# Kernel tuning notes

Measured on AMD Instinct MI355X. Metric: run time of the kernel, lower is better.

Reference implementation:

```python
import jax, jax.numpy as jnp
import numpy as np

EPS = 1e-7  # Keras binary_crossentropy epsilon


def setup_inputs() -> dict:
    key = jax.random.key(0)
    ks = jax.random.split(key, 4)
    B, D, H = 256, 512, 512
    return {
        "embeddings": jax.random.normal(ks[0], (B, D), dtype=jnp.float32),
        "labels": jax.random.randint(ks[1], (B,), 0, 16),
        "W1": jax.random.normal(ks[2], (2 * D, H), dtype=jnp.float32) / np.float32(np.sqrt(2 * D)),
        "b1": jnp.zeros((H,), jnp.float32),
        "W2": jax.random.normal(ks[3], (H, 1), dtype=jnp.float32) / np.float32(np.sqrt(H)),
        "b2": jnp.zeros((1,), jnp.float32),
    }


def reference(embeddings, labels, W1, b1, W2, b2):
    # All-pairs expansion equivalent to tf.meshgrid + tf.gather over batch indices.
    # Pair (i, j): input1 = embeddings[j] (fast axis), input2 = embeddings[i].
    B, D = embeddings.shape
    x1 = jnp.broadcast_to(embeddings[None, :, :], (B, B, D))
    x2 = jnp.broadcast_to(embeddings[:, None, :], (B, B, D))
    x = jnp.concatenate([x1, x2], axis=-1)  # (B, B, 2D)
    # metric_layer: siamese dense head -> pairwise similarity probability
    h = jax.nn.relu(jnp.einsum('ijd,dh->ijh', x, W1) + b1)          # (B, B, H)
    p = jax.nn.sigmoid(jnp.einsum('ijh,ho->ijo', h, W2) + b2)[..., 0]  # (B, B)
    p = jnp.clip(p, EPS, 1.0 - EPS)
    # target_function: label equality (symmetric, so pair order is irrelevant)
    t = (labels[:, None] == labels[None, :]).astype(p.dtype)        # (B, B)
    # loss: element-wise binary crossentropy over all B^2 pairs
    loss = -(t * jnp.log(p) + (1.0 - t) * jnp.log1p(-p))
    return loss.reshape(-1)  # (B*B,)
```

## Files before the change

### kernel.cpp

```cpp
#include <hip/hip_runtime.h>
#include <math.h>


#define B 256
#define D 512
#define H 512
#define KS 4
#define DC (D / KS)

__global__ __launch_bounds__(256) void head_partial(
    const float* __restrict__ emb, const float* __restrict__ W1,
    const float* __restrict__ b1, float* __restrict__ P) {
    __shared__ float sE[8 * DC];

    const int colhalf = blockIdx.x & 1;
    const int ks      = blockIdx.x >> 1;
    const int r0      = blockIdx.y * 8;
    const int z       = blockIdx.z;
    const int h       = colhalf * 256 + threadIdx.x;
    const int d0      = ks * DC;

    {
        const int r = threadIdx.x >> 5;
        const int c4 = threadIdx.x & 31;
        *(float4*)&sE[r * DC + c4 * 4] =
            *(const float4*)&emb[(size_t)(r0 + r) * D + d0 + c4 * 4];
    }
    __syncthreads();

    float acc[8];
    const float binit = (z == 0 && ks == 0) ? b1[h] : 0.0f;
#pragma unroll
    for (int r = 0; r < 8; ++r) acc[r] = binit;

    const float* w = W1 + (size_t)(z * D + d0) * H + h;

    float cur0 = w[0 * (size_t)H], cur1 = w[1 * (size_t)H];
    float cur2 = w[2 * (size_t)H], cur3 = w[3 * (size_t)H];
#pragma unroll 4
    for (int d = 0; d < DC; d += 4) {
        const int dn = (d + 4) & (DC - 1);
        const float n0 = w[(size_t)(dn + 0) * H];
        const float n1 = w[(size_t)(dn + 1) * H];
        const float n2 = w[(size_t)(dn + 2) * H];
        const float n3 = w[(size_t)(dn + 3) * H];
#pragma unroll
        for (int r = 0; r < 8; ++r) {
            float4 e = *(const float4*)&sE[r * DC + d];
            acc[r] = fmaf(e.x, cur0, acc[r]);
            acc[r] = fmaf(e.y, cur1, acc[r]);
            acc[r] = fmaf(e.z, cur2, acc[r]);
            acc[r] = fmaf(e.w, cur3, acc[r]);
        }
        cur0 = n0; cur1 = n1; cur2 = n2; cur3 = n3;
    }

    float* dst = P + ((size_t)(ks * 2 + z) * B + r0) * H + h;
#pragma unroll
    for (int r = 0; r < 8; ++r) dst[(size_t)r * H] = acc[r];
}

#define PADH 516

__global__ __launch_bounds__(128) void pair_loss(
    const float* __restrict__ P, const float* __restrict__ w2,
    const float* __restrict__ b2, const int* __restrict__ labels,
    float* __restrict__ out) {
    __shared__ float sA[16][PADH];
    __shared__ float sC[16][PADH];

    const int j0 = blockIdx.x * 16;
    const int i0 = blockIdx.y * 16;
    const int tid = threadIdx.x;
    const size_t KSTR = (size_t)2 * B * H;

    for (int idx = tid; idx < 16 * (H / 4); idx += 128) {
        const int r = idx >> 7;
        const int c4 = idx & 127;
        const float* pa = P + (size_t)(j0 + r) * H + c4 * 4;
        const float* pc = P + (size_t)(B + i0 + r) * H + c4 * 4;
        float4 a0 = *(const float4*)(pa);
        float4 a1 = *(const float4*)(pa + KSTR);
        float4 a2 = *(const float4*)(pa + 2 * KSTR);
        float4 a3 = *(const float4*)(pa + 3 * KSTR);
        float4 c0 = *(const float4*)(pc);
        float4 c1 = *(const float4*)(pc + KSTR);
        float4 c2 = *(const float4*)(pc + 2 * KSTR);
        float4 c3 = *(const float4*)(pc + 3 * KSTR);
        float4 va, vc;
        va.x = (a0.x + a1.x) + (a2.x + a3.x);
        va.y = (a0.y + a1.y) + (a2.y + a3.y);
        va.z = (a0.z + a1.z) + (a2.z + a3.z);
        va.w = (a0.w + a1.w) + (a2.w + a3.w);
        vc.x = (c0.x + c1.x) + (c2.x + c3.x);
        vc.y = (c0.y + c1.y) + (c2.y + c3.y);
        vc.z = (c0.z + c1.z) + (c2.z + c3.z);
        vc.w = (c0.w + c1.w) + (c2.w + c3.w);
        *(float4*)&sA[r][c4 * 4] = va;
        *(float4*)&sC[r][c4 * 4] = vc;
    }
    __syncthreads();

    const int tx = tid & 15;
    const int ty = tid >> 4;

    float s0 = 0.0f, s1 = 0.0f;
#pragma unroll 4
    for (int h = 0; h < H; h += 4) {
        float4 a  = *(const float4*)&sA[tx][h];
        float4 c0 = *(const float4*)&sC[ty][h];
        float4 c1 = *(const float4*)&sC[ty + 8][h];
        float4 w  = *(const float4*)&w2[h];
        s0 = fmaf(fmaxf(a.x + c0.x, 0.0f), w.x, s0);
        s0 = fmaf(fmaxf(a.y + c0.y, 0.0f), w.y, s0);
        s0 = fmaf(fmaxf(a.z + c0.z, 0.0f), w.z, s0);
        s0 = fmaf(fmaxf(a.w + c0.w, 0.0f), w.w, s0);
        s1 = fmaf(fmaxf(a.x + c1.x, 0.0f), w.x, s1);
        s1 = fmaf(fmaxf(a.y + c1.y, 0.0f), w.y, s1);
        s1 = fmaf(fmaxf(a.z + c1.z, 0.0f), w.z, s1);
        s1 = fmaf(fmaxf(a.w + c1.w, 0.0f), w.w, s1);
    }

    const float bias = b2[0];
    const int j = j0 + tx;
    const int lj = labels[j];

#pragma unroll
    for (int q = 0; q < 2; ++q) {
        const int i = i0 + ty + q * 8;
        const float z = (q ? s1 : s0) + bias;
        float p = 1.0f / (1.0f + expf(-z));
        p = fminf(fmaxf(p, 1e-7f), 1.0f - 1e-7f);
        const float t = (labels[i] == lj) ? 1.0f : 0.0f;
        const float loss = -(t * logf(p) + (1.0f - t) * log1pf(-p));
        out[(size_t)i * B + j] = loss;
    }
}

extern "C" void kernel_launch(void* const* d_in, const int* in_sizes, int n_in,
                              void* d_out, int out_size, void* d_ws, size_t ws_size,
                              hipStream_t stream) {
    const float* emb    = (const float*)d_in[0];
    const int*   labels = (const int*)d_in[1];
    const float* W1     = (const float*)d_in[2];
    const float* b1     = (const float*)d_in[3];
    const float* W2     = (const float*)d_in[4];
    const float* b2     = (const float*)d_in[5];
    float* out = (float*)d_out;

    float* P = (float*)d_ws;

    dim3 g1(2 * KS, 32, 2);
    head_partial<<<g1, 256, 0, stream>>>(emb, W1, b1, P);

    dim3 g2(16, 16);
    pair_loss<<<g2, 128, 0, stream>>>(P, W2, b2, labels, out);
}
```

Before: 33.94 us.

## Retile head projection so each wave computes 2 rows by 8 columns with float4 weight loads

The first-layer partial-projection kernel is retiled. Each thread now owns 2 embedding rows by 8 hidden columns, loaded as two float4 vectors of W1, instead of 8 rows by one scalar column. The grid is halved in x and the partial-sum buffer is relaid out by (z, ks) chunk, with the pair kernel's strides updated to match. The goal is wider, vectorised weight loads and float4 stores. The cost is that each W1 element is now reused across 2 rows per load instead of 8, so more W1 traffic goes through L2, and there are half as many blocks.

```diff
diff --git a/kernel.cpp b/kernel.cpp
--- a/kernel.cpp
+++ b/kernel.cpp
@@ -7,57 +7,82 @@
 #define H 512
 #define KS 4
 #define DC (D / KS)
+#define ROWS_H (B * H)
+
+__device__ __forceinline__ float4 fma4(float s, float4 w, float4 a) {
+    a.x = fmaf(s, w.x, a.x);
+    a.y = fmaf(s, w.y, a.y);
+    a.z = fmaf(s, w.z, a.z);
+    a.w = fmaf(s, w.w, a.w);
+    return a;
+}
 
 __global__ __launch_bounds__(256) void head_partial(
     const float* __restrict__ emb, const float* __restrict__ W1,
     const float* __restrict__ b1, float* __restrict__ P) {
     __shared__ float sE[8 * DC];
 
-    const int colhalf = blockIdx.x & 1;
-    const int ks      = blockIdx.x >> 1;
-    const int r0      = blockIdx.y * 8;
-    const int z       = blockIdx.z;
-    const int h       = colhalf * 256 + threadIdx.x;
-    const int d0      = ks * DC;
+    const int ks = blockIdx.x;
+    const int r0 = blockIdx.y * 8;
+    const int z  = blockIdx.z;
+    const int d0 = ks * DC;
 
     {
-        const int r = threadIdx.x >> 5;
+        const int r  = threadIdx.x >> 5;
         const int c4 = threadIdx.x & 31;
         *(float4*)&sE[r * DC + c4 * 4] =
             *(const float4*)&emb[(size_t)(r0 + r) * D + d0 + c4 * 4];
     }
     __syncthreads();
 
-    float acc[8];
-    const float binit = (z == 0 && ks == 0) ? b1[h] : 0.0f;
-#pragma unroll
-    for (int r = 0; r < 8; ++r) acc[r] = binit;
+    const int wave = threadIdx.x >> 6;
+    const int lane = threadIdx.x & 63;
+    const int hb   = 4 * lane;
 
-    const float* w = W1 + (size_t)(z * D + d0) * H + h;
-
-    float cur0 = w[0 * (size_t)H], cur1 = w[1 * (size_t)H];
-    float cur2 = w[2 * (size_t)H], cur3 = w[3 * (size_t)H];
-#pragma unroll 4
-    for (int d = 0; d < DC; d += 4) {
-        const int dn = (d + 4) & (DC - 1);
-        const float n0 = w[(size_t)(dn + 0) * H];
-        const float n1 = w[(size_t)(dn + 1) * H];
-        const float n2 = w[(size_t)(dn + 2) * H];
-        const float n3 = w[(size_t)(dn + 3) * H];
-#pragma unroll
-        for (int r = 0; r < 8; ++r) {
-            float4 e = *(const float4*)&sE[r * DC + d];
-            acc[r] = fmaf(e.x, cur0, acc[r]);
-            acc[r] = fmaf(e.y, cur1, acc[r]);
-            acc[r] = fmaf(e.z, cur2, acc[r]);
-            acc[r] = fmaf(e.w, cur3, acc[r]);
-        }
-        cur0 = n0; cur1 = n1; cur2 = n2; cur3 = n3;
+    float4 acc[2][2];
+    if (z == 0 && ks == 0) {
+        const float4 b0 = *(const float4*)&b1[hb];
+        const float4 bk = *(const float4*)&b1[256 + hb];
+        acc[0][0] = b0; acc[1][0] = b0;
+        acc[0][1] = bk; acc[1][1] = bk;
+    } else {
+        const float4 zf = make_float4(0.f, 0.f, 0.f, 0.f);
+        acc[0][0] = zf; acc[0][1] = zf; acc[1][0] = zf; acc[1][1] = zf;
     }
 
-    float* dst = P + ((size_t)(ks * 2 + z) * B + r0) * H + h;
+    const float* wp = W1 + (size_t)(z * D + d0) * H + hb;
+    const float* eb = sE + (2 * wave) * DC;
+
+#pragma unroll 2
+    for (int d = 0; d < DC; d += 4) {
+        float4 wv[4][2];
 #pragma unroll
-    for (int r = 0; r < 8; ++r) dst[(size_t)r * H] = acc[r];
+        for (int dd = 0; dd < 4; ++dd) {
+            const float* wr = wp + (size_t)(d + dd) * H;
+            wv[dd][0] = *(const float4*)wr;
+            wv[dd][1] = *(const float4*)(wr + 256);
+        }
+#pragma unroll
+        for (int r = 0; r < 2; ++r) {
+            const float4 e = *(const float4*)&eb[r * DC + d];
+            acc[r][0] = fma4(e.x, wv[0][0], acc[r][0]);
+            acc[r][1] = fma4(e.x, wv[0][1], acc[r][1]);
+            acc[r][0] = fma4(e.y, wv[1][0], acc[r][0]);
+            acc[r][1] = fma4(e.y, wv[1][1], acc[r][1]);
+            acc[r][0] = fma4(e.z, wv[2][0], acc[r][0]);
+            acc[r][1] = fma4(e.z, wv[2][1], acc[r][1]);
+            acc[r][0] = fma4(e.w, wv[3][0], acc[r][0]);
+            acc[r][1] = fma4(e.w, wv[3][1], acc[r][1]);
+        }
+    }
+
+    float* chunk = P + (size_t)(z * KS + ks) * ROWS_H;
+#pragma unroll
+    for (int r = 0; r < 2; ++r) {
+        float* dst = chunk + (size_t)(r0 + 2 * wave + r) * H + hb;
+        *(float4*)&dst[0]   = acc[r][0];
+        *(float4*)&dst[256] = acc[r][1];
+    }
 }
 
 #define PADH 516
@@ -72,21 +97,21 @@
     const int j0 = blockIdx.x * 16;
     const int i0 = blockIdx.y * 16;
     const int tid = threadIdx.x;
-    const size_t KSTR = (size_t)2 * B * H;
+    const size_t CSTR = (size_t)ROWS_H;
 
     for (int idx = tid; idx < 16 * (H / 4); idx += 128) {
         const int r = idx >> 7;
         const int c4 = idx & 127;
         const float* pa = P + (size_t)(j0 + r) * H + c4 * 4;
-        const float* pc = P + (size_t)(B + i0 + r) * H + c4 * 4;
+        const float* pc = P + KS * CSTR + (size_t)(i0 + r) * H + c4 * 4;
         float4 a0 = *(const float4*)(pa);
-        float4 a1 = *(const float4*)(pa + KSTR);
-        float4 a2 = *(const float4*)(pa + 2 * KSTR);
-        float4 a3 = *(const float4*)(pa + 3 * KSTR);
+        float4 a1 = *(const float4*)(pa + CSTR);
+        float4 a2 = *(const float4*)(pa + 2 * CSTR);
+        float4 a3 = *(const float4*)(pa + 3 * CSTR);
         float4 c0 = *(const float4*)(pc);
-        float4 c1 = *(const float4*)(pc + KSTR);
-        float4 c2 = *(const float4*)(pc + 2 * KSTR);
-        float4 c3 = *(const float4*)(pc + 3 * KSTR);
+        float4 c1 = *(const float4*)(pc + CSTR);
+        float4 c2 = *(const float4*)(pc + 2 * CSTR);
+        float4 c3 = *(const float4*)(pc + 3 * CSTR);
         float4 va, vc;
         va.x = (a0.x + a1.x) + (a2.x + a3.x);
         va.y = (a0.y + a1.y) + (a2.y + a3.y);
@@ -150,7 +175,7 @@
 
     float* P = (float*)d_ws;
 
-    dim3 g1(2 * KS, 32, 2);
+    dim3 g1(KS, 32, 2);
     head_partial<<<g1, 256, 0, stream>>>(emb, W1, b1, P);
 
     dim3 g2(16, 16);
```

New measurement: 36.79 us. 8.4% more time.
